# Kernel tuning notes

Hardware: AMD Instinct MI355X
Metric: run time of the kernel (lower is better)

Reference implementation:

```python
import jax, jax.numpy as jnp
import numpy as np

B, D, U = 4096, 1024, 1024

def cumax(a):
    # Faithful to source: softmax over last axis, cumsum over axis 0 (TF defaults).
    return jnp.cumsum(jax.nn.softmax(a, axis=-1), axis=0)

def setup_inputs() -> dict:
    key = jax.random.key(0)
    ks = jax.random.split(key, 21)
    names = ['inputs', 'hidden_prev', 'cell_prev',
             'Wf', 'Uf', 'bf', 'Wi', 'Ui', 'bi', 'Wo', 'Uo', 'bo',
             'Wc', 'Uc', 'bc', 'Wft', 'Uft', 'bft', 'Wit', 'Uit', 'bit']
    shapes = [(B, D), (B, U), (B, U)] + [(D, U), (U, U), (U,)] * 6
    scales = [1.0, 1.0, 1.0] + [0.05, 0.05, 0.05] * 6  # random_normal init ~ small stddev
    return {n: jax.random.normal(k, s, dtype=jnp.float32) * sc
            for n, k, s, sc in zip(names, ks, shapes, scales)}

def reference(inputs, hidden_prev, cell_prev,
              Wf, Uf, bf, Wi, Ui, bi, Wo, Uo, bo,
              Wc, Uc, bc, Wft, Uft, bft, Wit, Uit, bit):
    # Fuse the 12 small GEMMs into 2 big ones: [B,D]@[D,6U] and [B,U]@[U,6U]
    W_all = jnp.concatenate([Wf, Wi, Wo, Wc, Wft, Wit], axis=1)   # [D, 6U]
    U_all = jnp.concatenate([Uf, Ui, Uo, Uc, Uft, Uit], axis=1)   # [U, 6U]
    b_all = jnp.concatenate([bf, bi, bo, bc, bft, bit], axis=0)   # [6U]
    pre = inputs @ W_all + hidden_prev @ U_all + b_all            # [B, 6U]
    zf, zi, zo, zc, zft, zit = [pre[:, j*U:(j+1)*U] for j in range(6)]

    f = jax.nn.sigmoid(zf)
    i = jax.nn.sigmoid(zi)
    o = jax.nn.sigmoid(zo)
    c_hat = jnp.tanh(zc)
    f_tilde = cumax(zft)
    i_tilde = 1.0 - cumax(zit)

    omega = f_tilde * i_tilde
    f_hat = f * omega + (f_tilde - omega)
    i_hat = i * omega + (i_tilde - omega)
    cell = f_hat * cell_prev + i_hat * c_hat
    hidden = o * jnp.tanh(cell)
    return hidden, cell
```

## Files before the change

kernel.cpp:

```cpp
#include <hip/hip_runtime.h>
#include <cstdint>
#include <cstddef>


typedef _Float16 half8  __attribute__((ext_vector_type(8)));
typedef _Float16 half4v __attribute__((ext_vector_type(4)));
typedef float f32x4 __attribute__((ext_vector_type(4)));

__device__ __forceinline__ void async16(const _Float16* g, _Float16* l) {
  __builtin_amdgcn_global_load_lds(
      (const __attribute__((address_space(1))) void*)g,
      (__attribute__((address_space(3))) void*)l, 16, 0, 0);
}

struct Ptrs12 { const float* p[12]; };
struct Ptrs6  { const float* p[6];  };

__global__ void prep(const float* __restrict__ X, const float* __restrict__ H,
                     Ptrs12 w, Ptrs6 bs,
                     _Float16* __restrict__ Ahi, _Float16* __restrict__ Bhi,
                     float* __restrict__ b_all) {
  __shared__ float tile[64][65];
  const int blk = blockIdx.x;
  const int t = threadIdx.x;
  if (blk < 8192) {
    size_t base = ((size_t)blk * 256 + t) * 4;
    int k = (int)(base & 2047);
    size_t b = base >> 11;
    const float* src = (k < 1024) ? (X + b * 1024 + k) : (H + b * 1024 + (k - 1024));
    float4 v = *(const float4*)src;
    half4v hi = { (_Float16)v.x, (_Float16)v.y, (_Float16)v.z, (_Float16)v.w };
    *(half4v*)(Ahi + base) = hi;
  } else if (blk < 11264) {
    int bb = blk - 8192;
    int mat = bb >> 8;
    int tl = bb & 255;
    int tr = tl >> 4, tc = tl & 15;
    int g = mat >> 1, s = mat & 1;
    const float* src = w.p[mat];
    int col = t & 63, r0 = t >> 6;
#pragma unroll
    for (int i = 0; i < 16; i++) {
      int row = i * 4 + r0;
      tile[row][col] = src[(size_t)(tr * 64 + row) * 1024 + tc * 64 + col];
    }
    __syncthreads();
    int c2 = t >> 2, kseg = t & 3;
    half8 v0, v1;
#pragma unroll
    for (int j = 0; j < 8; j++) {
      v0[j] = (_Float16)(tile[kseg * 16 + j][c2] * 64.0f);
      v1[j] = (_Float16)(tile[kseg * 16 + 8 + j][c2] * 64.0f);
    }
    size_t n  = (size_t)g * 1024 + tc * 64 + c2;
    size_t kk = (size_t)s * 1024 + tr * 64 + kseg * 16;
    *(half8*)(Bhi + n * 2048 + kk) = v0;
    *(half8*)(Bhi + n * 2048 + kk + 8) = v1;
  } else {
    int n = (blk - 11264) * 256 + t;
    b_all[n] = bs.p[n >> 10][n & 1023];
  }
}

__global__ __launch_bounds__(256) void gemm_split(
    const _Float16* __restrict__ Ah, const _Float16* __restrict__ Bh,
    const float* __restrict__ b_all,
    _Float16* __restrict__ preG, float* __restrict__ preS) {
  __shared__ _Float16 lds[8192];
  _Float16* sAh = lds;
  _Float16* sBh = lds + 4096;

  const int pid = blockIdx.x;
  const int group = pid / (8 * 48);
  const int rem = pid % (8 * 48);
  const int mTile = group * 8 + (rem & 7);
  const int nTile = rem >> 3;

  const int t = threadIdx.x;
  const int lane = t & 63;
  const int wave = t >> 6;
  const int waveM = wave >> 1, waveN = wave & 1;
  const int kgrp = lane >> 4, frow = lane & 15;
  const size_t baseA = (size_t)mTile * 128 * 2048;
  const size_t baseB = (size_t)nTile * 128 * 2048;

  f32x4 acc[4][4] = {};

  for (int ks = 0; ks < 64; ks++) {
    const int k0 = ks * 32;
#pragma unroll
    for (int q = 0; q < 2; q++) {
      int slot = q * 256 + t;
      int r = slot >> 2;
      int sg = slot & 3;
      int sig = sg ^ ((r >> 1) & 3);
      size_t go = (size_t)r * 2048 + k0 + sig * 8;
      async16(Ah + baseA + go, sAh + slot * 8);
      async16(Bh + baseB + go, sBh + slot * 8);
    }
    __syncthreads();

    half8 ah[4], bh[4];
#pragma unroll
    for (int mi = 0; mi < 4; mi++) {
      int r = waveM * 64 + mi * 16 + frow;
      int ps = kgrp ^ ((r >> 1) & 3);
      ah[mi] = *(const half8*)(sAh + r * 32 + ps * 8);
    }
#pragma unroll
    for (int ni = 0; ni < 4; ni++) {
      int r = waveN * 64 + ni * 16 + frow;
      int ps = kgrp ^ ((r >> 1) & 3);
      bh[ni] = *(const half8*)(sBh + r * 32 + ps * 8);
    }
#pragma unroll
    for (int mi = 0; mi < 4; mi++)
#pragma unroll
      for (int ni = 0; ni < 4; ni++)
        acc[mi][ni] = __builtin_amdgcn_mfma_f32_16x16x32_f16(ah[mi], bh[ni], acc[mi][ni], 0, 0, 0);
    __syncthreads();
  }

  if (nTile < 32) {
#pragma unroll
    for (int ni = 0; ni < 4; ni++) {
      int col = nTile * 128 + waveN * 64 + ni * 16 + frow;
      float bias = b_all[col];
#pragma unroll
      for (int mi = 0; mi < 4; mi++) {
        int rbase = mTile * 128 + waveM * 64 + mi * 16 + kgrp * 4;
#pragma unroll
        for (int j = 0; j < 4; j++)
          preG[(size_t)(rbase + j) * 4096 + col] =
              (_Float16)(acc[mi][ni][j] * (1.0f / 64.0f) + bias);
      }
    }
  } else {
#pragma unroll
    for (int ni = 0; ni < 4; ni++) {
      int col = (nTile - 32) * 128 + waveN * 64 + ni * 16 + frow;
      float bias = b_all[4096 + col];
#pragma unroll
      for (int mi = 0; mi < 4; mi++) {
        int rbase = mTile * 128 + waveM * 64 + mi * 16 + kgrp * 4;
#pragma unroll
        for (int j = 0; j < 4; j++)
          preS[(size_t)(rbase + j) * 2048 + col] =
              acc[mi][ni][j] * (1.0f / 64.0f) + bias;
      }
    }
  }
}

__global__ void softmax_partials(const float* __restrict__ preS,
                                 _Float16* __restrict__ P, f32x4* __restrict__ part4) {
  __shared__ float wsum[4][1024];
  int m = blockIdx.x >> 9;
  int ch = blockIdx.x & 511;
  int t = threadIdx.x;
  int wave = t >> 6, lane = t & 63;
  f32x4 colacc[4] = {};
  for (int rr = 0; rr < 2; rr++) {
    int b = ch * 8 + wave * 2 + rr;
    const float* row = preS + (size_t)b * 2048 + m * 1024;
    _Float16* prow = P + ((size_t)m * 4096 + b) * 1024;
    f32x4 v[4];
    float mx = -3.4e38f;
#pragma unroll
    for (int j = 0; j < 4; j++) {
      v[j] = *(const f32x4*)(row + lane * 4 + 256 * j);
      mx = fmaxf(mx, fmaxf(fmaxf(v[j][0], v[j][1]), fmaxf(v[j][2], v[j][3])));
    }
#pragma unroll
    for (int off = 32; off > 0; off >>= 1) mx = fmaxf(mx, __shfl_xor(mx, off, 64));
    float sum = 0.f;
#pragma unroll
    for (int j = 0; j < 4; j++)
#pragma unroll
      for (int q = 0; q < 4; q++) { v[j][q] = __expf(v[j][q] - mx); sum += v[j][q]; }
#pragma unroll
    for (int off = 32; off > 0; off >>= 1) sum += __shfl_xor(sum, off, 64);
    float inv = 1.f / sum;
#pragma unroll
    for (int j = 0; j < 4; j++) {
      v[j] *= inv;
      half4v h = { (_Float16)v[j][0], (_Float16)v[j][1], (_Float16)v[j][2], (_Float16)v[j][3] };
      *(half4v*)(prow + lane * 4 + 256 * j) = h;
      colacc[j] += v[j];
    }
  }
#pragma unroll
  for (int j = 0; j < 4; j++)
    *(f32x4*)(&wsum[wave][lane * 4 + 256 * j]) = colacc[j];
  __syncthreads();
  f32x4 s = *(const f32x4*)(&wsum[0][t * 4]);
  s += *(const f32x4*)(&wsum[1][t * 4]);
  s += *(const f32x4*)(&wsum[2][t * 4]);
  s += *(const f32x4*)(&wsum[3][t * 4]);
  part4[((size_t)m * 256 + t) * 512 + ch] = s;
}

__global__ void scan_partials(const f32x4* __restrict__ part4, f32x4* __restrict__ off4) {
  int gidx = blockIdx.x * 4 + (threadIdx.x >> 6);
  int lane = threadIdx.x & 63;
  size_t base = (size_t)gidx * 512;
  f32x4 v[8];
  f32x4 s = {};
#pragma unroll
  for (int j = 0; j < 8; j++) {
    v[j] = part4[base + lane * 8 + j];
    s += v[j];
  }
  f32x4 incl = s;
#pragma unroll
  for (int off = 1; off < 64; off <<= 1) {
    f32x4 o;
#pragma unroll
    for (int q = 0; q < 4; q++) o[q] = __shfl_up(incl[q], off, 64);
    if (lane >= off) incl += o;
  }
  f32x4 run = incl - s;
#pragma unroll
  for (int j = 0; j < 8; j++) {
    off4[base + lane * 8 + j] = run;
    run += v[j];
  }
}

__global__ void onlstm_final(const _Float16* __restrict__ preG, const _Float16* __restrict__ P,
                             const float* __restrict__ cprev, const f32x4* __restrict__ off4,
                             float* __restrict__ out) {
  int ch = blockIdx.x;
  int c4 = threadIdx.x;
  int c = c4 * 4;
  f32x4 runf = off4[(size_t)c4 * 512 + ch];
  f32x4 runi = off4[(size_t)(256 + c4) * 512 + ch];
  for (int r = 0; r < 8; r++) {
    int b = ch * 8 + r;
    const _Float16* grow = preG + (size_t)b * 4096;
    half4v zf = *(const half4v*)(grow + c);
    half4v zi = *(const half4v*)(grow + 1024 + c);
    half4v zo = *(const half4v*)(grow + 2048 + c);
    half4v zc = *(const half4v*)(grow + 3072 + c);
    half4v pf = *(const half4v*)(P + (size_t)b * 1024 + c);
    half4v pi = *(const half4v*)(P + (size_t)(4096 + b) * 1024 + c);
    f32x4 cp = *(const f32x4*)(cprev + (size_t)b * 1024 + c);
    f32x4 hid, cel;
#pragma unroll
    for (int q = 0; q < 4; q++) {
      runf[q] += (float)pf[q];
      runi[q] += (float)pi[q];
      float ft = runf[q], it = 1.f - runi[q];
      float f  = 1.f / (1.f + __expf(-(float)zf[q]));
      float ii = 1.f / (1.f + __expf(-(float)zi[q]));
      float o  = 1.f / (1.f + __expf(-(float)zo[q]));
      float chat = tanhf((float)zc[q]);
      float omega = ft * it;
      float fhat = f * omega + (ft - omega);
      float ihat = ii * omega + (it - omega);
      float cell = fhat * cp[q] + ihat * chat;
      hid[q] = o * tanhf(cell);
      cel[q] = cell;
    }
    *(f32x4*)(out + (size_t)b * 1024 + c) = hid;
    *(f32x4*)(out + (size_t)4194304 + (size_t)b * 1024 + c) = cel;
  }
}

extern "C" void kernel_launch(void* const* d_in, const int* in_sizes, int n_in,
                              void* d_out, int out_size, void* d_ws, size_t ws_size,
                              hipStream_t stream) {
  const float* X = (const float*)d_in[0];
  const float* H = (const float*)d_in[1];
  const float* C = (const float*)d_in[2];

  char* ws = (char*)d_ws;
  _Float16* preG  = (_Float16*)(ws);
  float*    preS  = (float*)(ws + 33554432);
  _Float16* Ahi   = (_Float16*)(ws + 67108864);
  _Float16* Bhi   = (_Float16*)(ws + 83886080);
  _Float16* P     = (_Float16*)(ws + 109051904);
  float*    b_all = (float*)(ws + 125829120);
  f32x4*    part4 = (f32x4*)(ws + 125853696);
  f32x4*    off4  = (f32x4*)(ws + 130048000);

  Ptrs12 w;
  for (int g = 0; g < 6; g++) {
    w.p[2 * g]     = (const float*)d_in[3 + 3 * g];
    w.p[2 * g + 1] = (const float*)d_in[4 + 3 * g];
  }
  Ptrs6 bs;
  for (int g = 0; g < 6; g++) bs.p[g] = (const float*)d_in[5 + 3 * g];

  prep<<<11288, 256, 0, stream>>>(X, H, w, bs, Ahi, Bhi, b_all);
  gemm_split<<<1536, 256, 0, stream>>>(Ahi, Bhi, b_all, preG, preS);
  softmax_partials<<<1024, 256, 0, stream>>>(preS, P, part4);
  scan_partials<<<128, 256, 0, stream>>>(part4, off4);
  onlstm_final<<<512, 256, 0, stream>>>(preG, P, C, off4, (float*)d_out);
}
```

Baseline: 344.8 us.

## Unify pre-activations into one fp16 buffer with LDS-staged coalesced GEMM stores

The GEMM epilogue now stages each 64-row half of the output tile through LDS with a padded stride and writes 16-byte coalesced rows, instead of scattered 2-byte and 4-byte stores. All six gate pre-activations, including the softmax inputs, are kept in a single fp16 [B,6U] buffer. The softmax kernel overwrites that buffer in place with its probabilities, which removes the separate fp32 preS and P buffers. This cuts HBM traffic and store inefficiency, at the cost of fp16 precision for the softmax logits and extra LDS passes and syncs in the epilogue.

```diff
diff --git a/kernel.cpp b/kernel.cpp
--- a/kernel.cpp
+++ b/kernel.cpp
@@ -64,9 +64,8 @@
 
 __global__ __launch_bounds__(256) void gemm_split(
     const _Float16* __restrict__ Ah, const _Float16* __restrict__ Bh,
-    const float* __restrict__ b_all,
-    _Float16* __restrict__ preG, float* __restrict__ preS) {
-  __shared__ _Float16 lds[8192];
+    const float* __restrict__ b_all, _Float16* __restrict__ pre16) {
+  __shared__ _Float16 lds[64 * 136];
   _Float16* sAh = lds;
   _Float16* sBh = lds + 4096;
 
@@ -121,39 +120,41 @@
     __syncthreads();
   }
 
-  if (nTile < 32) {
-#pragma unroll
-    for (int ni = 0; ni < 4; ni++) {
-      int col = nTile * 128 + waveN * 64 + ni * 16 + frow;
-      float bias = b_all[col];
-#pragma unroll
-      for (int mi = 0; mi < 4; mi++) {
-        int rbase = mTile * 128 + waveM * 64 + mi * 16 + kgrp * 4;
-#pragma unroll
-        for (int j = 0; j < 4; j++)
-          preG[(size_t)(rbase + j) * 4096 + col] =
-              (_Float16)(acc[mi][ni][j] * (1.0f / 64.0f) + bias);
-      }
-    }
-  } else {
-#pragma unroll
-    for (int ni = 0; ni < 4; ni++) {
-      int col = (nTile - 32) * 128 + waveN * 64 + ni * 16 + frow;
-      float bias = b_all[4096 + col];
-#pragma unroll
-      for (int mi = 0; mi < 4; mi++) {
-        int rbase = mTile * 128 + waveM * 64 + mi * 16 + kgrp * 4;
-#pragma unroll
-        for (int j = 0; j < 4; j++)
-          preS[(size_t)(rbase + j) * 2048 + col] =
-              acc[mi][ni][j] * (1.0f / 64.0f) + bias;
-      }
-    }
-  }
-}
-
-__global__ void softmax_partials(const float* __restrict__ preS,
-                                 _Float16* __restrict__ P, f32x4* __restrict__ part4) {
+  const int cbase = nTile * 128;
+  float bias[4];
+#pragma unroll
+  for (int ni = 0; ni < 4; ni++)
+    bias[ni] = b_all[cbase + waveN * 64 + ni * 16 + frow];
+
+#pragma unroll
+  for (int pass = 0; pass < 2; pass++) {
+    if (waveM == pass) {
+#pragma unroll
+      for (int mi = 0; mi < 4; mi++)
+#pragma unroll
+        for (int ni = 0; ni < 4; ni++) {
+          int colL = waveN * 64 + ni * 16 + frow;
+#pragma unroll
+          for (int j = 0; j < 4; j++) {
+            int rowL = mi * 16 + kgrp * 4 + j;
+            lds[rowL * 136 + colL] =
+                (_Float16)(acc[mi][ni][j] * (1.0f / 64.0f) + bias[ni]);
+          }
+        }
+    }
+    __syncthreads();
+#pragma unroll
+    for (int rnd = 0; rnd < 4; rnd++) {
+      int row = rnd * 16 + (t >> 4);
+      int seg = t & 15;
+      half8 v = *(const half8*)(lds + row * 136 + seg * 8);
+      *(half8*)(pre16 + (size_t)(mTile * 128 + pass * 64 + row) * 6144 + cbase + seg * 8) = v;
+    }
+    __syncthreads();
+  }
+}
+
+__global__ void softmax_partials(_Float16* __restrict__ pre16, f32x4* __restrict__ part4) {
   __shared__ float wsum[4][1024];
   int m = blockIdx.x >> 9;
   int ch = blockIdx.x & 511;
@@ -162,13 +163,13 @@
   f32x4 colacc[4] = {};
   for (int rr = 0; rr < 2; rr++) {
     int b = ch * 8 + wave * 2 + rr;
-    const float* row = preS + (size_t)b * 2048 + m * 1024;
-    _Float16* prow = P + ((size_t)m * 4096 + b) * 1024;
+    _Float16* row = pre16 + (size_t)b * 6144 + (4 + m) * 1024;
     f32x4 v[4];
     float mx = -3.4e38f;
 #pragma unroll
     for (int j = 0; j < 4; j++) {
-      v[j] = *(const f32x4*)(row + lane * 4 + 256 * j);
+      half4v h = *(const half4v*)(row + lane * 4 + 256 * j);
+      v[j] = f32x4{ (float)h[0], (float)h[1], (float)h[2], (float)h[3] };
       mx = fmaxf(mx, fmaxf(fmaxf(v[j][0], v[j][1]), fmaxf(v[j][2], v[j][3])));
     }
 #pragma unroll
@@ -185,7 +186,7 @@
     for (int j = 0; j < 4; j++) {
       v[j] *= inv;
       half4v h = { (_Float16)v[j][0], (_Float16)v[j][1], (_Float16)v[j][2], (_Float16)v[j][3] };
-      *(half4v*)(prow + lane * 4 + 256 * j) = h;
+      *(half4v*)(row + lane * 4 + 256 * j) = h;
       colacc[j] += v[j];
     }
   }
@@ -227,7 +228,7 @@
   }
 }
 
-__global__ void onlstm_final(const _Float16* __restrict__ preG, const _Float16* __restrict__ P,
+__global__ void onlstm_final(const _Float16* __restrict__ pre16,
                              const float* __restrict__ cprev, const f32x4* __restrict__ off4,
                              float* __restrict__ out) {
   int ch = blockIdx.x;
@@ -237,13 +238,13 @@
   f32x4 runi = off4[(size_t)(256 + c4) * 512 + ch];
   for (int r = 0; r < 8; r++) {
     int b = ch * 8 + r;
-    const _Float16* grow = preG + (size_t)b * 4096;
-    half4v zf = *(const half4v*)(grow + c);
-    half4v zi = *(const half4v*)(grow + 1024 + c);
-    half4v zo = *(const half4v*)(grow + 2048 + c);
-    half4v zc = *(const half4v*)(grow + 3072 + c);
-    half4v pf = *(const half4v*)(P + (size_t)b * 1024 + c);
-    half4v pi = *(const half4v*)(P + (size_t)(4096 + b) * 1024 + c);
+    const _Float16* row = pre16 + (size_t)b * 6144;
+    half4v zf = *(const half4v*)(row + c);
+    half4v zi = *(const half4v*)(row + 1024 + c);
+    half4v zo = *(const half4v*)(row + 2048 + c);
+    half4v zc = *(const half4v*)(row + 3072 + c);
+    half4v pf = *(const half4v*)(row + 4096 + c);
+    half4v pi = *(const half4v*)(row + 5120 + c);
     f32x4 cp = *(const f32x4*)(cprev + (size_t)b * 1024 + c);
     f32x4 hid, cel;
 #pragma unroll
@@ -275,14 +276,12 @@
   const float* C = (const float*)d_in[2];
 
   char* ws = (char*)d_ws;
-  _Float16* preG  = (_Float16*)(ws);
-  float*    preS  = (float*)(ws + 33554432);
-  _Float16* Ahi   = (_Float16*)(ws + 67108864);
-  _Float16* Bhi   = (_Float16*)(ws + 83886080);
-  _Float16* P     = (_Float16*)(ws + 109051904);
-  float*    b_all = (float*)(ws + 125829120);
-  f32x4*    part4 = (f32x4*)(ws + 125853696);
-  f32x4*    off4  = (f32x4*)(ws + 130048000);
+  _Float16* pre16 = (_Float16*)(ws);
+  _Float16* Ahi   = (_Float16*)(ws + 50331648);
+  _Float16* Bhi   = (_Float16*)(ws + 67108864);
+  float*    b_all = (float*)(ws + 92274688);
+  f32x4*    part4 = (f32x4*)(ws + 92299264);
+  f32x4*    off4  = (f32x4*)(ws + 96493568);
 
   Ptrs12 w;
   for (int g = 0; g < 6; g++) {
@@ -293,8 +292,8 @@
   for (int g = 0; g < 6; g++) bs.p[g] = (const float*)d_in[5 + 3 * g];
 
   prep<<<11288, 256, 0, stream>>>(X, H, w, bs, Ahi, Bhi, b_all);
-  gemm_split<<<1536, 256, 0, stream>>>(Ahi, Bhi, b_all, preG, preS);
-  softmax_partials<<<1024, 256, 0, stream>>>(preS, P, part4);
+  gemm_split<<<1536, 256, 0, stream>>>(Ahi, Bhi, b_all, pre16);
+  softmax_partials<<<1024, 256, 0, stream>>>(pre16, part4);
   scan_partials<<<128, 256, 0, stream>>>(part4, off4);
-  onlstm_final<<<512, 256, 0, stream>>>(preG, P, C, off4, (float*)d_out);
-}
+  onlstm_final<<<512, 256, 0, stream>>>(pre16, C, off4, (float*)d_out);
+}
```

Measured after the change: 332.3 us. 3.6% less time.
